# Optimization experiments

Hardware: AMD Instinct MI355X
Metric: run time of the kernel (lower is better)

The kernel has to match this reference:

```python
import jax, jax.numpy as jnp
import numpy as np

B, C, N, Hdim, Wdim = 32, 64, 16384, 128, 128  # N = Hdim*Wdim, C = dim = num_embeddings
EPS = 1e-5


def setup_inputs() -> dict:
    key = jax.random.key(0)
    ks = jax.random.split(key, 6)
    s = 0.05  # weight scale
    return {
        "x": jax.random.normal(ks[0], (B, C, N), dtype=jnp.float32),
        "Wq": jax.random.normal(ks[1], (C, C), dtype=jnp.float32) * s,   # Conv1d q (1x1)
        "bq": jnp.zeros((C,), jnp.float32),
        "gamma": jnp.ones((C,), jnp.float32),                              # BatchNorm1d affine
        "beta": jnp.zeros((C,), jnp.float32),
        "Wq2": jax.random.normal(ks[2], (C, C), dtype=jnp.float32) * s,  # Conv1d q2 (1x1)
        "bq2": jnp.zeros((C,), jnp.float32),
        "Wsr": jax.random.normal(ks[3], (C, C), dtype=jnp.float32) * s,  # Conv2d sr, k=1,s=1 -> 1x1
        "bsr": jnp.zeros((C,), jnp.float32),
        "Wc": jax.random.normal(ks[4], (C, C), dtype=jnp.float32) * s,   # Conv1d conv (1x1, no bias)
        "H": Hdim,
        "W": Wdim,
    }


def reference(x, Wq, bq, gamma, beta, Wq2, bq2, Wsr, bsr, Wc, H, W):
    # x: (B, C, N), N = H*W, sr_ratio = 1
    # q = q2(BN(q(x))) -- all 1x1 convs; BN uses batch statistics (torch training mode)
    q = jnp.einsum('oc,bcn->bon', Wq, x) + bq[None, :, None]            # (B,C,N)
    mu = q.mean(axis=(0, 2), keepdims=True)
    var = q.var(axis=(0, 2), keepdims=True)
    q = (q - mu) * jax.lax.rsqrt(var + EPS)
    q = q * gamma[None, :, None] + beta[None, :, None]
    q = jnp.einsum('oc,bcn->bon', Wq2, q) + bq2[None, :, None]          # (B,C,N)

    # k = sr(x) with kernel/stride 1 -> 1x1 conv, then permute to (B,N,C)
    k = jnp.einsum('oc,bcn->bon', Wsr, x) + bsr[None, :, None]          # (B,C,N)

    # v = AvgPool1d(C) over the channel axis of x^T -> channel mean, (B,1,N)
    v = x.mean(axis=1, keepdims=True)                                    # (B,1,N)

    # attn = q @ k^T over the N axis -> (B,C,C), then MaxPool1d(C) -> row-wise max (B,C,1)
    attn = jnp.einsum('bcn,bdn->bcd', q, k)                              # (B,C,C)
    attn = attn.max(axis=-1, keepdims=True)                              # (B,C,1)

    # out = conv( attn @ v )  -- outer product broadcast, then 1x1 conv (no bias)
    out = attn * v                                                       # (B,C,N)
    out = jnp.einsum('oc,bcn->bon', Wc, out)                             # (B,C,N)
    return out
```

## Files before the change

kernel.cpp:

```cpp
#include <hip/hip_runtime.h>
#include <hip/hip_bf16.h>

#define B_ 32
#define C_ 64
#define N_ 16384
constexpr float BN_INV = 1.0f / (32.0f * 16384.0f);

typedef float f32x4 __attribute__((ext_vector_type(4)));
typedef short s16x8 __attribute__((ext_vector_type(8)));

constexpr size_t WS_GPART = 0;
constexpr size_t WS_RPART = WS_GPART + (size_t)512 * 4096;
constexpr size_t WS_G     = WS_RPART + (size_t)512 * 64;
constexpr size_t WS_RB    = WS_G + (size_t)32 * 4096;
constexpr size_t WS_V     = WS_RB + (size_t)32 * 64;
constexpr size_t WS_W     = WS_V + (size_t)32 * N_;

__device__ constexpr int P1I[10] = {0,0,0,0,1,1,1,2,2,3};
__device__ constexpr int P1J[10] = {0,1,2,3,1,2,3,2,3,3};
__device__ constexpr int P1AT[4][4] = {{0,1,2,3},{1,4,5,6},{2,5,7,8},{3,6,8,9}};

__device__ __forceinline__ unsigned short bf16_rne_s(float f) {
    unsigned u = __float_as_uint(f);
    unsigned r = u + 0x7FFFu + ((u >> 16) & 1u);
    return (unsigned short)(r >> 16);
}
__device__ __forceinline__ void cvt8hi(const f32x4& a, const f32x4& b, s16x8& hi) {
    float f[8] = {a[0], a[1], a[2], a[3], b[0], b[1], b[2], b[3]};
    #pragma unroll
    for (int j = 0; j < 8; ++j) hi[j] = (short)bf16_rne_s(f[j]);
}

__global__ __launch_bounds__(512, 2) void k1(const float* __restrict__ x, float* __restrict__ ws) {
    __shared__ __align__(16) float rawb[4][10 * 256];
    __shared__ float rws[8][64];
    const int t = threadIdx.x, wv = t >> 6, lane = t & 63;
    const int b = blockIdx.x >> 4, ch = blockIdx.x & 15;
    const int kg = lane >> 4, cl = lane & 15;
    const float* xb = x + ((size_t)b * C_ + cl) * N_ + ch * 1024 + kg * 8;

    f32x4 accP1[10];
    #pragma unroll
    for (int i = 0; i < 10; ++i) accP1[i] = (f32x4){0.f, 0.f, 0.f, 0.f};
    f32x4 rs = {0.f, 0.f, 0.f, 0.f};

    f32x4 cA[4], cB[4], nA[4], nB[4];
    #pragma unroll
    for (int g = 0; g < 4; ++g) {
        cA[g] = *(const f32x4*)(xb + (size_t)g * (16 * N_) + wv * 32);
        cB[g] = *(const f32x4*)(xb + (size_t)g * (16 * N_) + wv * 32 + 4);
    }

    for (int w = 0; w < 4; ++w) {
        if (w < 3) {
            const int noff = (8 * (w + 1) + wv) * 32;
            #pragma unroll
            for (int g = 0; g < 4; ++g) {
                nA[g] = *(const f32x4*)(xb + (size_t)g * (16 * N_) + noff);
                nB[g] = *(const f32x4*)(xb + (size_t)g * (16 * N_) + noff + 4);
            }
        }
        s16x8 hi[4];
        #pragma unroll
        for (int g = 0; g < 4; ++g) cvt8hi(cA[g], cB[g], hi[g]);

        f32x4 s0 = cA[0] + cA[1] + cA[2] + cA[3];
        f32x4 s1 = cB[0] + cB[1] + cB[2] + cB[3];
        #pragma unroll
        for (int m = 1; m <= 8; m <<= 1) {
            #pragma unroll
            for (int j = 0; j < 4; ++j) {
                s0[j] += __shfl_xor(s0[j], m);
                s1[j] += __shfl_xor(s1[j], m);
            }
        }
        if (cl == 0) {
            float* vp = ws + WS_V + (size_t)b * N_ + ch * 1024 + (8 * w + wv) * 32 + kg * 8;
            *(f32x4*)vp       = s0 * 0.015625f;
            *(f32x4*)(vp + 4) = s1 * 0.015625f;
        }
        #pragma unroll
        for (int g = 0; g < 4; ++g)
            rs[g] += cA[g][0] + cA[g][1] + cA[g][2] + cA[g][3]
                   + cB[g][0] + cB[g][1] + cB[g][2] + cB[g][3];

        #pragma unroll
        for (int i = 0; i < 10; ++i)
            accP1[i] = __builtin_amdgcn_mfma_f32_16x16x32_bf16(hi[P1I[i]], hi[P1J[i]], accP1[i], 0, 0, 0);

        #pragma unroll
        for (int g = 0; g < 4; ++g) { cA[g] = nA[g]; cB[g] = nB[g]; }
    }

    #pragma unroll
    for (int g = 0; g < 4; ++g) {
        rs[g] += __shfl_xor(rs[g], 16);
        rs[g] += __shfl_xor(rs[g], 32);
    }
    if (lane < 16) {
        #pragma unroll
        for (int g = 0; g < 4; ++g) rws[wv][g * 16 + lane] = rs[g];
    }

    if (wv < 4) {
        float* dst = rawb[wv];
        #pragma unroll
        for (int i = 0; i < 10; ++i) *(f32x4*)(dst + i * 256 + lane * 4) = accP1[i];
    }
    __syncthreads();
    if (wv >= 4) {
        float* dst = rawb[wv - 4];
        #pragma unroll
        for (int i = 0; i < 10; ++i) {
            f32x4 o = *(f32x4*)(dst + i * 256 + lane * 4);
            *(f32x4*)(dst + i * 256 + lane * 4) = o + accP1[i];
        }
    }
    __syncthreads();
    if (t < 64) {
        float s = 0.f;
        #pragma unroll
        for (int g = 0; g < 8; ++g) s += rws[g][t];
        ws[WS_RPART + (size_t)blockIdx.x * 64 + t] = s;
    }
    float* gp = ws + WS_GPART + (size_t)blockIdx.x * 4096;
    for (int e = t; e < 4096; e += 512) {
        const int r = e >> 6, c = e & 63;
        const int bi = r >> 4, bj = c >> 4, rr = r & 15, cc = c & 15;
        const int i1 = P1AT[bi][bj] * 256;
        const int o1 = (bi <= bj) ? (((rr >> 2) * 16 + cc) * 4 + (rr & 3))
                                  : (((cc >> 2) * 16 + rr) * 4 + (cc & 3));
        gp[e] = rawb[0][i1 + o1] + rawb[1][i1 + o1] + rawb[2][i1 + o1] + rawb[3][i1 + o1];
    }
}

__global__ __launch_bounds__(256) void k2a(float* __restrict__ ws) {
    const int b = blockIdx.x >> 3, sl = blockIdx.x & 7, t = threadIdx.x;
    #pragma unroll
    for (int h = 0; h < 2; ++h) {
        const int e = sl * 512 + h * 256 + t;
        float s = 0.f;
        for (int chn = 0; chn < 16; ++chn) s += ws[WS_GPART + ((size_t)(b * 16 + chn)) * 4096 + e];
        ws[WS_G + (size_t)b * 4096 + e] = s;
    }
    if (sl == 0 && t < 64) {
        float s = 0.f;
        for (int chn = 0; chn < 16; ++chn) s += ws[WS_RPART + (size_t)(b * 16 + chn) * 64 + t];
        ws[WS_RB + b * 64 + t] = s;
    }
}

__global__ __launch_bounds__(256) void k2b(const float* __restrict__ Wq, const float* __restrict__ gamma,
                                           const float* __restrict__ beta, const float* __restrict__ Wq2,
                                           const float* __restrict__ bq2, const float* __restrict__ Wsr,
                                           const float* __restrict__ bsr, const float* __restrict__ Wc,
                                           float* __restrict__ ws) {
    __shared__ __align__(16) unsigned short OPH[3][64 * 72];
    __shared__ float F1[64 * 65], F2[64 * 65];
    __shared__ float mS[64], muS[64], DS[64], abv[64], quadS[64];
    __shared__ float rl[64], ul[64], avs[64], sbv[64], pls[64], aml[64];
    const int bb = blockIdx.x, t = threadIdx.x;
    const int w = t >> 6, lane = t & 63, cl = lane & 15, jg = lane >> 4;
    const int sr = t >> 2, sc0 = (t & 3) * 16;

    {
        f32x4 s[4];
        #pragma unroll
        for (int j = 0; j < 4; ++j) s[j] = (f32x4){0.f, 0.f, 0.f, 0.f};
        for (int b = 0; b < 32; ++b) {
            const float* gbp = ws + WS_G + (size_t)b * 4096 + sr * 64 + sc0;
            #pragma unroll
            for (int j = 0; j < 4; ++j) s[j] += *(const f32x4*)(gbp + 4 * j);
        }
        s16x8 h8[2];
        #pragma unroll
        for (int q = 0; q < 2; ++q)
            #pragma unroll
            for (int j = 0; j < 8; ++j)
                h8[q][j] = (short)bf16_rne_s(s[q * 2 + (j >> 2)][j & 3] * BN_INV);
        *(s16x8*)(&OPH[0][sr * 72 + sc0])     = h8[0];
        *(s16x8*)(&OPH[0][sr * 72 + sc0 + 8]) = h8[1];
    }
    #pragma unroll
    for (int mtx = 0; mtx < 2; ++mtx) {
        const float* src = (mtx == 0 ? Wq : Wq2) + sr * 64 + sc0;
        float* F = (mtx == 0) ? F1 : F2;
        s16x8 h8[2];
        #pragma unroll
        for (int q = 0; q < 2; ++q) {
            f32x4 a = *(const f32x4*)(src + q * 8);
            f32x4 b = *(const f32x4*)(src + q * 8 + 4);
            #pragma unroll
            for (int j = 0; j < 8; ++j) {
                float v = (j < 4) ? a[j] : b[j - 4];
                F[sr * 65 + sc0 + q * 8 + j] = v;
                h8[q][j] = (short)bf16_rne_s(v);
            }
        }
        unsigned short* H = OPH[1 + mtx];
        *(s16x8*)(&H[sr * 72 + sc0])     = h8[0];
        *(s16x8*)(&H[sr * 72 + sc0 + 8]) = h8[1];
    }
    if (t < 64) {
        float sm = 0.f;
        for (int b = 0; b < 32; ++b) sm += ws[WS_RB + b * 64 + t];
        mS[t] = sm * BN_INV;
        rl[t] = ws[WS_RB + bb * 64 + t];
        sbv[t] = bsr[t];
    }
    __syncthreads();

    auto mm64 = [&](const unsigned short* AH, const unsigned short* BH, f32x4 acc[4]) {
        #pragma unroll
        for (int ks = 0; ks < 2; ++ks) {
            const int ko = ks * 32 + jg * 8;
            s16x8 ah = *(const s16x8*)(AH + (16 * w + cl) * 72 + ko);
            #pragma unroll
            for (int bj = 0; bj < 4; ++bj) {
                s16x8 bh = *(const s16x8*)(BH + (16 * bj + cl) * 72 + ko);
                acc[bj] = __builtin_amdgcn_mfma_f32_16x16x32_bf16(ah, bh, acc[bj], 0, 0, 0);
            }
        }
    };

    {
        f32x4 acc[4];
        #pragma unroll
        for (int i = 0; i < 4; ++i) acc[i] = (f32x4){0.f, 0.f, 0.f, 0.f};
        mm64(OPH[1], OPH[0], acc);
        float s[4] = {0.f, 0.f, 0.f, 0.f};
        #pragma unroll
        for (int j = 0; j < 4; ++j) {
            const int row = 16 * w + jg * 4 + j;
            #pragma unroll
            for (int bj = 0; bj < 4; ++bj) s[j] += acc[bj][j] * F1[row * 65 + 16 * bj + cl];
        }
        #pragma unroll
        for (int m = 1; m <= 8; m <<= 1)
            #pragma unroll
            for (int j = 0; j < 4; ++j) s[j] += __shfl_xor(s[j], m);
        if (cl == 0) {
            #pragma unroll
            for (int j = 0; j < 4; ++j) quadS[16 * w + jg * 4 + j] = s[j];
        }
        if (t < 64) {
            float s2 = 0.f;
            for (int c = 0; c < 64; ++c) s2 += F1[t * 65 + c] * mS[c];
            muS[t] = s2;
        }
    }
    __syncthreads();

    if (t < 64) {
        const float var = quadS[t] - muS[t] * muS[t];
        const float D = gamma[t] * rsqrtf(var + 1e-5f);
        DS[t] = D;
        abv[t] = beta[t] - D * muS[t];
    }
    __syncthreads();
    {
        s16x8 h8[2];
        #pragma unroll
        for (int q = 0; q < 2; ++q)
            #pragma unroll
            for (int j = 0; j < 8; ++j) {
                const int c = sc0 + q * 8 + j;
                h8[q][j] = (short)bf16_rne_s(DS[c] * F1[c * 65 + sr]);
            }
        *(s16x8*)(&OPH[0][sr * 72 + sc0])     = h8[0];
        *(s16x8*)(&OPH[0][sr * 72 + sc0 + 8]) = h8[1];
    }
    if (t < 64) {
        float s = 0.f;
        for (int k = 0; k < 64; ++k) s += F2[t * 65 + k] * abv[k];
        avs[t] = s + bq2[t];
    }
    __syncthreads();

    {
        f32x4 acc[4];
        #pragma unroll
        for (int i = 0; i < 4; ++i) acc[i] = (f32x4){0.f, 0.f, 0.f, 0.f};
        mm64(OPH[2], OPH[0], acc);
        float s[4] = {0.f, 0.f, 0.f, 0.f};
        #pragma unroll
        for (int bj = 0; bj < 4; ++bj) {
            const float cv = rl[16 * bj + cl];
            #pragma unroll
            for (int j = 0; j < 4; ++j) s[j] += acc[bj][j] * cv;
        }
        #pragma unroll
        for (int m = 1; m <= 8; m <<= 1)
            #pragma unroll
            for (int j = 0; j < 4; ++j) s[j] += __shfl_xor(s[j], m);
        if (cl == 0) {
            #pragma unroll
            for (int j = 0; j < 4; ++j) ul[16 * w + jg * 4 + j] = s[j];
        }
        #pragma unroll
        for (int bj = 0; bj < 4; ++bj)
            #pragma unroll
            for (int j = 0; j < 4; ++j) {
                const int row = 16 * w + jg * 4 + j, col = 16 * bj + cl;
                OPH[1][row * 72 + col] = (unsigned short)bf16_rne_s(acc[bj][j]);
            }
    }
    __syncthreads();

    {
        const float* gbp = ws + WS_G + (size_t)bb * 4096 + sr * 64 + sc0;
        s16x8 h8[2];
        #pragma unroll
        for (int q = 0; q < 2; ++q) {
            f32x4 a = *(const f32x4*)(gbp + q * 8);
            f32x4 b = *(const f32x4*)(gbp + q * 8 + 4);
            #pragma unroll
            for (int j = 0; j < 8; ++j)
                h8[q][j] = (short)bf16_rne_s((j < 4) ? a[j] : b[j - 4]);
        }
        *(s16x8*)(&OPH[0][sr * 72 + sc0])     = h8[0];
        *(s16x8*)(&OPH[0][sr * 72 + sc0 + 8]) = h8[1];
        const float* ssrc = Wsr + sr * 64 + sc0;
        #pragma unroll
        for (int q = 0; q < 2; ++q) {
            f32x4 a = *(const f32x4*)(ssrc + q * 8);
            f32x4 b = *(const f32x4*)(ssrc + q * 8 + 4);
            #pragma unroll
            for (int j = 0; j < 8; ++j) {
                float v = (j < 4) ? a[j] : b[j - 4];
                F1[sr * 65 + sc0 + q * 8 + j] = v;
                h8[q][j] = (short)bf16_rne_s(v);
            }
        }
        *(s16x8*)(&OPH[2][sr * 72 + sc0])     = h8[0];
        *(s16x8*)(&OPH[2][sr * 72 + sc0 + 8]) = h8[1];
    }
    __syncthreads();

    f32x4 accT[4];
    #pragma unroll
    for (int i = 0; i < 4; ++i) accT[i] = (f32x4){0.f, 0.f, 0.f, 0.f};
    if (t < 64) {
        float s = 0.f;
        for (int k = 0; k < 64; ++k) s += F1[t * 65 + k] * rl[k];
        pls[t] = s + 16384.f * sbv[t];
    }
    mm64(OPH[1], OPH[0], accT);
    __syncthreads();
    #pragma unroll
    for (int bj = 0; bj < 4; ++bj)
        #pragma unroll
        for (int j = 0; j < 4; ++j) {
            const int row = 16 * w + jg * 4 + j, col = 16 * bj + cl;
            OPH[0][row * 72 + col] = (unsigned short)bf16_rne_s(accT[bj][j]);
        }
    __syncthreads();

    {
        f32x4 acc[4];
        #pragma unroll
        for (int i = 0; i < 4; ++i) acc[i] = (f32x4){0.f, 0.f, 0.f, 0.f};
        mm64(OPH[0], OPH[2], acc);
        float mx[4] = {-3.4e38f, -3.4e38f, -3.4e38f, -3.4e38f};
        #pragma unroll
        for (int j = 0; j < 4; ++j) {
            const int row = 16 * w + jg * 4 + j;
            const float ur = ul[row], ar = avs[row];
            #pragma unroll
            for (int bj = 0; bj < 4; ++bj) {
                const int col = 16 * bj + cl;
                const float v = acc[bj][j] + ur * sbv[col] + ar * pls[col];
                mx[j] = fmaxf(mx[j], v);
            }
        }
        #pragma unroll
        for (int m = 1; m <= 8; m <<= 1)
            #pragma unroll
            for (int j = 0; j < 4; ++j) mx[j] = fmaxf(mx[j], __shfl_xor(mx[j], m));
        if (cl == 0) {
            #pragma unroll
            for (int j = 0; j < 4; ++j) aml[16 * w + jg * 4 + j] = mx[j];
        }
    }
    __syncthreads();

    if (t < 64) {
        float s = 0.f;
        for (int c = 0; c < 64; ++c) s += Wc[t * 64 + c] * aml[c];
        ws[WS_W + bb * 64 + t] = s;
    }
}

__global__ __launch_bounds__(256) void k3(const float* __restrict__ ws, float* __restrict__ out) {
    const int blk = blockIdx.x;
    const int b = blk >> 6, seg = blk & 63;
    const int r0 = (seg >> 4) * 16, chk = seg & 15;
    __shared__ float wls[16];
    const int t = threadIdx.x;
    if (t < 16) wls[t] = ws[WS_W + b * 64 + r0 + t];
    __syncthreads();
    const size_t nb = (size_t)chk * 1024 + 4 * t;
    const f32x4 v4 = *(const f32x4*)(ws + WS_V + (size_t)b * N_ + nb);
    float* ob = out + ((size_t)b * C_ + r0) * N_ + nb;
    #pragma unroll
    for (int o = 0; o < 16; ++o) {
        __builtin_nontemporal_store(v4 * wls[o], (f32x4*)(ob + (size_t)o * N_));
    }
}

extern "C" void kernel_launch(void* const* d_in, const int* in_sizes, int n_in,
                              void* d_out, int out_size, void* d_ws, size_t ws_size,
                              hipStream_t stream) {
    const float* x     = (const float*)d_in[0];
    const float* Wq    = (const float*)d_in[1];
    const float* gamma = (const float*)d_in[3];
    const float* beta  = (const float*)d_in[4];
    const float* Wq2   = (const float*)d_in[5];
    const float* bq2   = (const float*)d_in[6];
    const float* Wsr   = (const float*)d_in[7];
    const float* bsr   = (const float*)d_in[8];
    const float* Wc    = (const float*)d_in[9];
    float* ws  = (float*)d_ws;
    float* out = (float*)d_out;

    hipLaunchKernelGGL(k1,  dim3(512),  dim3(512), 0, stream, x, ws);
    hipLaunchKernelGGL(k2a, dim3(256),  dim3(256), 0, stream, ws);
    hipLaunchKernelGGL(k2b, dim3(32),   dim3(256), 0, stream,
                       Wq, gamma, beta, Wq2, bq2, Wsr, bsr, Wc, ws);
    hipLaunchKernelGGL(k3,  dim3(2048), dim3(256), 0, stream, ws, out);
}
```

Baseline: 75.36 us.

## Fuse four kernels into one cooperative persistent kernel with grid syncs

Replaces the four-kernel pipeline (Gram/row-sum pass, partial reduction, per-batch small-matrix stage, output broadcast) with a single cooperative kernel of 256 blocks separated by grid.sync barriers. Each block now covers twice as many columns in the first phase, and the final broadcast writes all 64 output rows per block with nontemporal stores. The aim is to remove launch gaps and inter-kernel tails. In exchange, only 32 of 256 blocks work during the small-matrix phase while the rest wait at the barrier, and the output write uses fewer, larger blocks. The old four-kernel path is kept as a fallback if the cooperative launch fails.

Result: slower. 294.1 us (+290.3%).

```diff
diff --git a/kernel.cpp b/kernel.cpp
--- a/kernel.cpp
+++ b/kernel.cpp
@@ -1,5 +1,8 @@
 #include <hip/hip_runtime.h>
 #include <hip/hip_bf16.h>
+#include <hip/hip_cooperative_groups.h>
+
+namespace cg = cooperative_groups;
 
 #define B_ 32
 #define C_ 64
@@ -31,6 +34,407 @@
     for (int j = 0; j < 8; ++j) hi[j] = (short)bf16_rne_s(f[j]);
 }
 
+__global__ __launch_bounds__(512, 2) void mega(const float* __restrict__ x,
+                                               const float* __restrict__ Wq,
+                                               const float* __restrict__ gamma,
+                                               const float* __restrict__ beta,
+                                               const float* __restrict__ Wq2,
+                                               const float* __restrict__ bq2,
+                                               const float* __restrict__ Wsr,
+                                               const float* __restrict__ bsr,
+                                               const float* __restrict__ Wc,
+                                               float* __restrict__ ws,
+                                               float* __restrict__ out) {
+    __shared__ __align__(16) unsigned char smem[63744];
+    cg::grid_group grid = cg::this_grid();
+    const int t = threadIdx.x;
+
+    {
+        float* rawbF = (float*)smem;
+        float* rwsF  = (float*)(smem + 40960);
+        const int wv = t >> 6, lane = t & 63;
+        const int b = blockIdx.x >> 3, ch8 = blockIdx.x & 7;
+        const int kg = lane >> 4, cl = lane & 15;
+        const float* xb = x + ((size_t)b * C_ + cl) * N_ + ch8 * 2048 + kg * 8;
+
+        f32x4 accP1[10];
+        #pragma unroll
+        for (int i = 0; i < 10; ++i) accP1[i] = (f32x4){0.f, 0.f, 0.f, 0.f};
+        f32x4 rs = {0.f, 0.f, 0.f, 0.f};
+
+        f32x4 cA[4], cB[4], nA[4], nB[4];
+        #pragma unroll
+        for (int g = 0; g < 4; ++g) {
+            cA[g] = *(const f32x4*)(xb + (size_t)g * (16 * N_) + wv * 32);
+            cB[g] = *(const f32x4*)(xb + (size_t)g * (16 * N_) + wv * 32 + 4);
+        }
+
+        for (int w = 0; w < 8; ++w) {
+            if (w < 7) {
+                const int noff = (8 * (w + 1) + wv) * 32;
+                #pragma unroll
+                for (int g = 0; g < 4; ++g) {
+                    nA[g] = *(const f32x4*)(xb + (size_t)g * (16 * N_) + noff);
+                    nB[g] = *(const f32x4*)(xb + (size_t)g * (16 * N_) + noff + 4);
+                }
+            }
+            s16x8 hi[4];
+            #pragma unroll
+            for (int g = 0; g < 4; ++g) cvt8hi(cA[g], cB[g], hi[g]);
+
+            f32x4 s0 = cA[0] + cA[1] + cA[2] + cA[3];
+            f32x4 s1 = cB[0] + cB[1] + cB[2] + cB[3];
+            #pragma unroll
+            for (int m = 1; m <= 8; m <<= 1) {
+                #pragma unroll
+                for (int j = 0; j < 4; ++j) {
+                    s0[j] += __shfl_xor(s0[j], m);
+                    s1[j] += __shfl_xor(s1[j], m);
+                }
+            }
+            if (cl == 0) {
+                float* vp = ws + WS_V + (size_t)b * N_ + ch8 * 2048 + (8 * w + wv) * 32 + kg * 8;
+                *(f32x4*)vp       = s0 * 0.015625f;
+                *(f32x4*)(vp + 4) = s1 * 0.015625f;
+            }
+            #pragma unroll
+            for (int g = 0; g < 4; ++g)
+                rs[g] += cA[g][0] + cA[g][1] + cA[g][2] + cA[g][3]
+                       + cB[g][0] + cB[g][1] + cB[g][2] + cB[g][3];
+
+            #pragma unroll
+            for (int i = 0; i < 10; ++i)
+                accP1[i] = __builtin_amdgcn_mfma_f32_16x16x32_bf16(hi[P1I[i]], hi[P1J[i]], accP1[i], 0, 0, 0);
+
+            #pragma unroll
+            for (int g = 0; g < 4; ++g) { cA[g] = nA[g]; cB[g] = nB[g]; }
+        }
+
+        #pragma unroll
+        for (int g = 0; g < 4; ++g) {
+            rs[g] += __shfl_xor(rs[g], 16);
+            rs[g] += __shfl_xor(rs[g], 32);
+        }
+        if (lane < 16) {
+            #pragma unroll
+            for (int g = 0; g < 4; ++g) rwsF[wv * 64 + g * 16 + lane] = rs[g];
+        }
+
+        if (wv < 4) {
+            float* dst = rawbF + wv * 2560;
+            #pragma unroll
+            for (int i = 0; i < 10; ++i) *(f32x4*)(dst + i * 256 + lane * 4) = accP1[i];
+        }
+        __syncthreads();
+        if (wv >= 4) {
+            float* dst = rawbF + (wv - 4) * 2560;
+            #pragma unroll
+            for (int i = 0; i < 10; ++i) {
+                f32x4 o = *(f32x4*)(dst + i * 256 + lane * 4);
+                *(f32x4*)(dst + i * 256 + lane * 4) = o + accP1[i];
+            }
+        }
+        __syncthreads();
+        if (t < 64) {
+            float s = 0.f;
+            #pragma unroll
+            for (int g = 0; g < 8; ++g) s += rwsF[g * 64 + t];
+            ws[WS_RPART + (size_t)blockIdx.x * 64 + t] = s;
+        }
+        float* gp = ws + WS_GPART + (size_t)blockIdx.x * 4096;
+        for (int e = t; e < 4096; e += 512) {
+            const int r = e >> 6, c = e & 63;
+            const int bi = r >> 4, bj = c >> 4, rr = r & 15, cc = c & 15;
+            const int i1 = P1AT[bi][bj] * 256;
+            const int o1 = (bi <= bj) ? (((rr >> 2) * 16 + cc) * 4 + (rr & 3))
+                                      : (((cc >> 2) * 16 + rr) * 4 + (cc & 3));
+            gp[e] = rawbF[0 * 2560 + i1 + o1] + rawbF[1 * 2560 + i1 + o1]
+                  + rawbF[2 * 2560 + i1 + o1] + rawbF[3 * 2560 + i1 + o1];
+        }
+    }
+    __threadfence();
+    grid.sync();
+
+    {
+        const int b = blockIdx.x >> 3, sl = blockIdx.x & 7;
+        const int e = sl * 512 + t;
+        float s = 0.f;
+        #pragma unroll
+        for (int chn = 0; chn < 8; ++chn) s += ws[WS_GPART + ((size_t)(b * 8 + chn)) * 4096 + e];
+        ws[WS_G + (size_t)b * 4096 + e] = s;
+        if (sl == 0 && t < 64) {
+            float s2 = 0.f;
+            #pragma unroll
+            for (int chn = 0; chn < 8; ++chn) s2 += ws[WS_RPART + (size_t)(b * 8 + chn) * 64 + t];
+            ws[WS_RB + b * 64 + t] = s2;
+        }
+    }
+    __threadfence();
+    grid.sync();
+
+    if (blockIdx.x < 32) {
+        const int bb = blockIdx.x;
+        unsigned short* OPH0 = (unsigned short*)smem;
+        unsigned short* OPH1 = OPH0 + 64 * 72;
+        unsigned short* OPH2 = OPH1 + 64 * 72;
+        float* F1 = (float*)(smem + 27648);
+        float* F2 = (float*)(smem + 44288);
+        float* SV = (float*)(smem + 60928);
+        float *mS = SV, *muS = SV + 64, *DSv = SV + 128, *abv = SV + 192, *quadS = SV + 256,
+              *rl = SV + 320, *ul = SV + 384, *avs = SV + 448, *sbv = SV + 512,
+              *pls = SV + 576, *aml = SV + 640;
+        const int w = t >> 6, lane = t & 63, cl = lane & 15, jg = lane >> 4;
+        const int sr = t >> 2, sc0 = (t & 3) * 16;
+
+        if (t < 256) {
+            f32x4 s[4];
+            #pragma unroll
+            for (int j = 0; j < 4; ++j) s[j] = (f32x4){0.f, 0.f, 0.f, 0.f};
+            for (int b = 0; b < 32; ++b) {
+                const float* gbp = ws + WS_G + (size_t)b * 4096 + sr * 64 + sc0;
+                #pragma unroll
+                for (int j = 0; j < 4; ++j) s[j] += *(const f32x4*)(gbp + 4 * j);
+            }
+            s16x8 h8[2];
+            #pragma unroll
+            for (int q = 0; q < 2; ++q)
+                #pragma unroll
+                for (int j = 0; j < 8; ++j)
+                    h8[q][j] = (short)bf16_rne_s(s[q * 2 + (j >> 2)][j & 3] * BN_INV);
+            *(s16x8*)(&OPH0[sr * 72 + sc0])     = h8[0];
+            *(s16x8*)(&OPH0[sr * 72 + sc0 + 8]) = h8[1];
+            #pragma unroll
+            for (int mtx = 0; mtx < 2; ++mtx) {
+                const float* src = (mtx == 0 ? Wq : Wq2) + sr * 64 + sc0;
+                float* F = (mtx == 0) ? F1 : F2;
+                s16x8 g8[2];
+                #pragma unroll
+                for (int q = 0; q < 2; ++q) {
+                    f32x4 a = *(const f32x4*)(src + q * 8);
+                    f32x4 b = *(const f32x4*)(src + q * 8 + 4);
+                    #pragma unroll
+                    for (int j = 0; j < 8; ++j) {
+                        float v = (j < 4) ? a[j] : b[j - 4];
+                        F[sr * 65 + sc0 + q * 8 + j] = v;
+                        g8[q][j] = (short)bf16_rne_s(v);
+                    }
+                }
+                unsigned short* H = (mtx == 0) ? OPH1 : OPH2;
+                *(s16x8*)(&H[sr * 72 + sc0])     = g8[0];
+                *(s16x8*)(&H[sr * 72 + sc0 + 8]) = g8[1];
+            }
+        }
+        if (t < 64) {
+            float sm = 0.f;
+            for (int b = 0; b < 32; ++b) sm += ws[WS_RB + b * 64 + t];
+            mS[t] = sm * BN_INV;
+            rl[t] = ws[WS_RB + bb * 64 + t];
+            sbv[t] = bsr[t];
+        }
+        __syncthreads();
+
+        auto mm64 = [&](const unsigned short* AH, const unsigned short* BH, f32x4 acc[4]) {
+            #pragma unroll
+            for (int ks = 0; ks < 2; ++ks) {
+                const int ko = ks * 32 + jg * 8;
+                s16x8 ah = *(const s16x8*)(AH + (16 * w + cl) * 72 + ko);
+                #pragma unroll
+                for (int bj = 0; bj < 4; ++bj) {
+                    s16x8 bh = *(const s16x8*)(BH + (16 * bj + cl) * 72 + ko);
+                    acc[bj] = __builtin_amdgcn_mfma_f32_16x16x32_bf16(ah, bh, acc[bj], 0, 0, 0);
+                }
+            }
+        };
+
+        if (t < 256) {
+            f32x4 acc[4];
+            #pragma unroll
+            for (int i = 0; i < 4; ++i) acc[i] = (f32x4){0.f, 0.f, 0.f, 0.f};
+            mm64(OPH1, OPH0, acc);
+            float s[4] = {0.f, 0.f, 0.f, 0.f};
+            #pragma unroll
+            for (int j = 0; j < 4; ++j) {
+                const int row = 16 * w + jg * 4 + j;
+                #pragma unroll
+                for (int bj = 0; bj < 4; ++bj) s[j] += acc[bj][j] * F1[row * 65 + 16 * bj + cl];
+            }
+            #pragma unroll
+            for (int m = 1; m <= 8; m <<= 1)
+                #pragma unroll
+                for (int j = 0; j < 4; ++j) s[j] += __shfl_xor(s[j], m);
+            if (cl == 0) {
+                #pragma unroll
+                for (int j = 0; j < 4; ++j) quadS[16 * w + jg * 4 + j] = s[j];
+            }
+            if (t < 64) {
+                float s2 = 0.f;
+                for (int c = 0; c < 64; ++c) s2 += F1[t * 65 + c] * mS[c];
+                muS[t] = s2;
+            }
+        }
+        __syncthreads();
+
+        if (t < 64) {
+            const float var = quadS[t] - muS[t] * muS[t];
+            const float D = gamma[t] * rsqrtf(var + 1e-5f);
+            DSv[t] = D;
+            abv[t] = beta[t] - D * muS[t];
+        }
+        __syncthreads();
+        if (t < 256) {
+            s16x8 h8[2];
+            #pragma unroll
+            for (int q = 0; q < 2; ++q)
+                #pragma unroll
+                for (int j = 0; j < 8; ++j) {
+                    const int c = sc0 + q * 8 + j;
+                    h8[q][j] = (short)bf16_rne_s(DSv[c] * F1[c * 65 + sr]);
+                }
+            *(s16x8*)(&OPH0[sr * 72 + sc0])     = h8[0];
+            *(s16x8*)(&OPH0[sr * 72 + sc0 + 8]) = h8[1];
+            if (t < 64) {
+                float s = 0.f;
+                for (int k = 0; k < 64; ++k) s += F2[t * 65 + k] * abv[k];
+                avs[t] = s + bq2[t];
+            }
+        }
+        __syncthreads();
+
+        if (t < 256) {
+            f32x4 acc[4];
+            #pragma unroll
+            for (int i = 0; i < 4; ++i) acc[i] = (f32x4){0.f, 0.f, 0.f, 0.f};
+            mm64(OPH2, OPH0, acc);
+            float s[4] = {0.f, 0.f, 0.f, 0.f};
+            #pragma unroll
+            for (int bj = 0; bj < 4; ++bj) {
+                const float cv = rl[16 * bj + cl];
+                #pragma unroll
+                for (int j = 0; j < 4; ++j) s[j] += acc[bj][j] * cv;
+            }
+            #pragma unroll
+            for (int m = 1; m <= 8; m <<= 1)
+                #pragma unroll
+                for (int j = 0; j < 4; ++j) s[j] += __shfl_xor(s[j], m);
+            if (cl == 0) {
+                #pragma unroll
+                for (int j = 0; j < 4; ++j) ul[16 * w + jg * 4 + j] = s[j];
+            }
+            #pragma unroll
+            for (int bj = 0; bj < 4; ++bj)
+                #pragma unroll
+                for (int j = 0; j < 4; ++j) {
+                    const int row = 16 * w + jg * 4 + j, col = 16 * bj + cl;
+                    OPH1[row * 72 + col] = (unsigned short)bf16_rne_s(acc[bj][j]);
+                }
+        }
+        __syncthreads();
+
+        if (t < 256) {
+            const float* gbp = ws + WS_G + (size_t)bb * 4096 + sr * 64 + sc0;
+            s16x8 h8[2];
+            #pragma unroll
+            for (int q = 0; q < 2; ++q) {
+                f32x4 a = *(const f32x4*)(gbp + q * 8);
+                f32x4 b = *(const f32x4*)(gbp + q * 8 + 4);
+                #pragma unroll
+                for (int j = 0; j < 8; ++j)
+                    h8[q][j] = (short)bf16_rne_s((j < 4) ? a[j] : b[j - 4]);
+            }
+            *(s16x8*)(&OPH0[sr * 72 + sc0])     = h8[0];
+            *(s16x8*)(&OPH0[sr * 72 + sc0 + 8]) = h8[1];
+            const float* ssrc = Wsr + sr * 64 + sc0;
+            #pragma unroll
+            for (int q = 0; q < 2; ++q) {
+                f32x4 a = *(const f32x4*)(ssrc + q * 8);
+                f32x4 b = *(const f32x4*)(ssrc + q * 8 + 4);
+                #pragma unroll
+                for (int j = 0; j < 8; ++j) {
+                    float v = (j < 4) ? a[j] : b[j - 4];
+                    F1[sr * 65 + sc0 + q * 8 + j] = v;
+                    h8[q][j] = (short)bf16_rne_s(v);
+                }
+            }
+            *(s16x8*)(&OPH2[sr * 72 + sc0])     = h8[0];
+            *(s16x8*)(&OPH2[sr * 72 + sc0 + 8]) = h8[1];
+        }
+        __syncthreads();
+
+        f32x4 accT[4];
+        if (t < 256) {
+            #pragma unroll
+            for (int i = 0; i < 4; ++i) accT[i] = (f32x4){0.f, 0.f, 0.f, 0.f};
+            if (t < 64) {
+                float s = 0.f;
+                for (int k = 0; k < 64; ++k) s += F1[t * 65 + k] * rl[k];
+                pls[t] = s + 16384.f * sbv[t];
+            }
+            mm64(OPH1, OPH0, accT);
+        }
+        __syncthreads();
+        if (t < 256) {
+            #pragma unroll
+            for (int bj = 0; bj < 4; ++bj)
+                #pragma unroll
+                for (int j = 0; j < 4; ++j) {
+                    const int row = 16 * w + jg * 4 + j, col = 16 * bj + cl;
+                    OPH0[row * 72 + col] = (unsigned short)bf16_rne_s(accT[bj][j]);
+                }
+        }
+        __syncthreads();
+
+        if (t < 256) {
+            f32x4 acc[4];
+            #pragma unroll
+            for (int i = 0; i < 4; ++i) acc[i] = (f32x4){0.f, 0.f, 0.f, 0.f};
+            mm64(OPH0, OPH2, acc);
+            float mx[4] = {-3.4e38f, -3.4e38f, -3.4e38f, -3.4e38f};
+            #pragma unroll
+            for (int j = 0; j < 4; ++j) {
+                const int row = 16 * w + jg * 4 + j;
+                const float ur = ul[row], ar = avs[row];
+                #pragma unroll
+                for (int bj = 0; bj < 4; ++bj) {
+                    const int col = 16 * bj + cl;
+                    const float v = acc[bj][j] + ur * sbv[col] + ar * pls[col];
+                    mx[j] = fmaxf(mx[j], v);
+                }
+            }
+            #pragma unroll
+            for (int m = 1; m <= 8; m <<= 1)
+                #pragma unroll
+                for (int j = 0; j < 4; ++j) mx[j] = fmaxf(mx[j], __shfl_xor(mx[j], m));
+            if (cl == 0) {
+                #pragma unroll
+                for (int j = 0; j < 4; ++j) aml[16 * w + jg * 4 + j] = mx[j];
+            }
+        }
+        __syncthreads();
+
+        if (t < 64) {
+            float s = 0.f;
+            for (int c = 0; c < 64; ++c) s += Wc[t * 64 + c] * aml[c];
+            ws[WS_W + bb * 64 + t] = s;
+        }
+    }
+    __threadfence();
+    grid.sync();
+
+    {
+        float* wls = (float*)smem;
+        const int b = blockIdx.x >> 3, ch8 = blockIdx.x & 7;
+        if (t < 64) wls[t] = ws[WS_W + b * 64 + t];
+        __syncthreads();
+        const size_t col = (size_t)ch8 * 2048 + (size_t)t * 4;
+        const f32x4 v4 = *(const f32x4*)(ws + WS_V + (size_t)b * N_ + col);
+        float* ob = out + (size_t)b * C_ * N_ + col;
+        #pragma unroll
+        for (int o = 0; o < 64; ++o) {
+            __builtin_nontemporal_store(v4 * wls[o], (f32x4*)(ob + (size_t)o * N_));
+        }
+    }
+}
+
 __global__ __launch_bounds__(512, 2) void k1(const float* __restrict__ x, float* __restrict__ ws) {
     __shared__ __align__(16) float rawb[4][10 * 256];
     __shared__ float rws[8][64];
@@ -50,7 +454,6 @@
         cA[g] = *(const f32x4*)(xb + (size_t)g * (16 * N_) + wv * 32);
         cB[g] = *(const f32x4*)(xb + (size_t)g * (16 * N_) + wv * 32 + 4);
     }
-
     for (int w = 0; w < 4; ++w) {
         if (w < 3) {
             const int noff = (8 * (w + 1) + wv) * 32;
@@ -63,7 +466,6 @@
         s16x8 hi[4];
         #pragma unroll
         for (int g = 0; g < 4; ++g) cvt8hi(cA[g], cB[g], hi[g]);
-
         f32x4 s0 = cA[0] + cA[1] + cA[2] + cA[3];
         f32x4 s1 = cB[0] + cB[1] + cB[2] + cB[3];
         #pragma unroll
@@ -83,15 +485,12 @@
         for (int g = 0; g < 4; ++g)
             rs[g] += cA[g][0] + cA[g][1] + cA[g][2] + cA[g][3]
                    + cB[g][0] + cB[g][1] + cB[g][2] + cB[g][3];
-
         #pragma unroll
         for (int i = 0; i < 10; ++i)
             accP1[i] = __builtin_amdgcn_mfma_f32_16x16x32_bf16(hi[P1I[i]], hi[P1J[i]], accP1[i], 0, 0, 0);
-
         #pragma unroll
         for (int g = 0; g < 4; ++g) { cA[g] = nA[g]; cB[g] = nB[g]; }
     }
-
     #pragma unroll
     for (int g = 0; g < 4; ++g) {
         rs[g] += __shfl_xor(rs[g], 16);
@@ -101,7 +500,6 @@
         #pragma unroll
         for (int g = 0; g < 4; ++g) rws[wv][g * 16 + lane] = rs[g];
     }
-
     if (wv < 4) {
         float* dst = rawb[wv];
         #pragma unroll
@@ -162,7 +560,6 @@
     const int bb = blockIdx.x, t = threadIdx.x;
     const int w = t >> 6, lane = t & 63, cl = lane & 15, jg = lane >> 4;
     const int sr = t >> 2, sc0 = (t & 3) * 16;
-
     {
         f32x4 s[4];
         #pragma unroll
@@ -209,7 +606,6 @@
         sbv[t] = bsr[t];
     }
     __syncthreads();
-
     auto mm64 = [&](const unsigned short* AH, const unsigned short* BH, f32x4 acc[4]) {
         #pragma unroll
         for (int ks = 0; ks < 2; ++ks) {
@@ -222,7 +618,6 @@
             }
         }
     };
-
     {
         f32x4 acc[4];
         #pragma unroll
@@ -250,7 +645,6 @@
         }
     }
     __syncthreads();
-
     if (t < 64) {
         const float var = quadS[t] - muS[t] * muS[t];
         const float D = gamma[t] * rsqrtf(var + 1e-5f);
@@ -276,7 +670,6 @@
         avs[t] = s + bq2[t];
     }
     __syncthreads();
-
     {
         f32x4 acc[4];
         #pragma unroll
@@ -306,7 +699,6 @@
             }
     }
     __syncthreads();
-
     {
         const float* gbp = ws + WS_G + (size_t)bb * 4096 + sr * 64 + sc0;
         s16x8 h8[2];
@@ -336,7 +728,6 @@
         *(s16x8*)(&OPH[2][sr * 72 + sc0 + 8]) = h8[1];
     }
     __syncthreads();
-
     f32x4 accT[4];
     #pragma unroll
     for (int i = 0; i < 4; ++i) accT[i] = (f32x4){0.f, 0.f, 0.f, 0.f};
@@ -355,7 +746,6 @@
             OPH[0][row * 72 + col] = (unsigned short)bf16_rne_s(accT[bj][j]);
         }
     __syncthreads();
-
     {
         f32x4 acc[4];
         #pragma unroll
@@ -383,7 +773,6 @@
         }
     }
     __syncthreads();
-
     if (t < 64) {
         float s = 0.f;
         for (int c = 0; c < 64; ++c) s += Wc[t * 64 + c] * aml[c];
@@ -423,9 +812,15 @@
     float* ws  = (float*)d_ws;
     float* out = (float*)d_out;
 
-    hipLaunchKernelGGL(k1,  dim3(512),  dim3(512), 0, stream, x, ws);
-    hipLaunchKernelGGL(k2a, dim3(256),  dim3(256), 0, stream, ws);
-    hipLaunchKernelGGL(k2b, dim3(32),   dim3(256), 0, stream,
-                       Wq, gamma, beta, Wq2, bq2, Wsr, bsr, Wc, ws);
-    hipLaunchKernelGGL(k3,  dim3(2048), dim3(256), 0, stream, ws, out);
+    void* args[] = {(void*)&x, (void*)&Wq, (void*)&gamma, (void*)&beta, (void*)&Wq2,
+                    (void*)&bq2, (void*)&Wsr, (void*)&bsr, (void*)&Wc, (void*)&ws, (void*)&out};
+    hipError_t err = hipLaunchCooperativeKernel((void*)mega, dim3(256), dim3(512), args, 0, stream);
+    if (err != hipSuccess) {
+        (void)hipGetLastError();
+        hipLaunchKernelGGL(k1,  dim3(512),  dim3(512), 0, stream, x, ws);
+        hipLaunchKernelGGL(k2a, dim3(256),  dim3(256), 0, stream, ws);
+        hipLaunchKernelGGL(k2b, dim3(32),   dim3(256), 0, stream,
+                           Wq, gamma, beta, Wq2, bq2, Wsr, bsr, Wc, ws);
+        hipLaunchKernelGGL(k3,  dim3(2048), dim3(256), 0, stream, ws, out);
+    }
 }
```
